# Kernel optimization log

Measured on AMD Instinct MI355X. Metric: run time of the kernel, lower is better.

The kernel has to match this reference:

```python
import jax, jax.numpy as jnp
import numpy as np

B, H, W, D, L, M = 16, 256, 256, 32, 4, 12  # batch, grid H, grid W, d_model, num_layers, modes
BN_EPS = 1e-5


def setup_inputs() -> dict:
    key = jax.random.key(0)
    ks = jax.random.split(key, 12)
    scale = 1.0 / (D * D)  # SpectralConv2d init scale: 1/(in_ch*out_ch)
    return {
        "x": jax.random.normal(ks[0], (B, H, W), jnp.float32),
        "coords_x": jax.random.uniform(ks[1], (1, 2, 1, H, W), dtype=jnp.float32),
        # linear_in: 3 -> D
        "w_in": jax.random.normal(ks[2], (D, 3), jnp.float32) * 0.3,
        "b_in": jnp.zeros((D,), jnp.float32),
        # per-layer spectral weights (real/imag), torch.rand-style uniform [0,1)*scale
        "w1r": jax.random.uniform(ks[3], (L, D, D, M, M), dtype=jnp.float32) * scale,
        "w1i": jax.random.uniform(ks[4], (L, D, D, M, M), dtype=jnp.float32) * scale,
        "w2r": jax.random.uniform(ks[5], (L, D, D, M, M), dtype=jnp.float32) * scale,
        "w2i": jax.random.uniform(ks[6], (L, D, D, M, M), dtype=jnp.float32) * scale,
        # per-layer pointwise linear D -> D
        "lw": jax.random.normal(ks[7], (L, D, D), jnp.float32) * (1.0 / np.sqrt(D)),
        "lb": jnp.zeros((L, D), jnp.float32),
        # per-layer BatchNorm affine params
        "gamma": jnp.ones((L, D), jnp.float32),
        "beta": jnp.zeros((L, D), jnp.float32),
        # linear_out: D -> 1
        "w_out": jax.random.normal(ks[8], (1, D), jnp.float32) * (1.0 / np.sqrt(D)),
        "b_out": jnp.zeros((1,), jnp.float32),
    }


def _fourier_layer(h, w1, w2, lw, lb, gamma, beta):
    # h: [B, D, H, W]
    Bh, C, Hh, Wh = h.shape
    h_ft = jnp.fft.rfft2(h)  # [B, D, H, W//2+1] complex64
    # low-mode truncation + complex channel mixing on two corner blocks
    top = jnp.einsum('bixy,ioxy->boxy', h_ft[:, :, :M, :M], w1)
    bot = jnp.einsum('bixy,ioxy->boxy', h_ft[:, :, Hh - M:, :M], w2)
    out_ft = jnp.zeros((Bh, C, Hh, Wh // 2 + 1), jnp.complex64)
    out_ft = out_ft.at[:, :, :M, :M].set(top).at[:, :, Hh - M:, :M].set(bot)
    y = jnp.fft.irfft2(out_ft, s=(Hh, Wh))  # [B, D, H, W]
    # residual pointwise linear (x + Linear(x)), then ReLU, then BatchNorm2d (batch stats)
    y = y + jnp.einsum('bchw,oc->bohw', y, lw) + lb[None, :, None, None]
    y = jax.nn.relu(y)
    mean = y.mean(axis=(0, 2, 3), keepdims=True)
    var = y.var(axis=(0, 2, 3), keepdims=True)
    y = (y - mean) * jax.lax.rsqrt(var + BN_EPS)
    return y * gamma[None, :, None, None] + beta[None, :, None, None]


def reference(x, coords_x, w_in, b_in, w1r, w1i, w2r, w2i, lw, lb, gamma, beta, w_out, b_out):
    # coords_x: [1,2,1,H,W] -> squeeze dim 2 -> broadcast to [B,2,H,W]
    cx = jnp.broadcast_to(coords_x[:, :, 0], (x.shape[0], 2, H, W))
    h = jnp.concatenate([x[:, None], cx], axis=1)  # [B, 3, H, W]
    h = jnp.einsum('bchw,dc->bdhw', h, w_in) + b_in[None, :, None, None]  # linear_in
    for i in range(L):  # fixed small layer count
        h = _fourier_layer(h, w1r[i] + 1j * w1i[i], w2r[i] + 1j * w2i[i],
                           lw[i], lb[i], gamma[i], beta[i])
    out = jnp.einsum('bdhw,od->bohw', h, w_out) + b_out[None, :, None, None]  # linear_out
    return out[:, 0]  # [B, H, W]
```

## Files before the change

kernel.cpp:

```cpp
#include <hip/hip_runtime.h>

constexpr double PI2 = 6.283185307179586476925286766559;
constexpr float INV_HW = 1.0f / 65536.0f;


__global__ __launch_bounds__(256) void k_init(float* __restrict__ cs,
                                              float* __restrict__ Tg) {
  int t = threadIdx.x;
  double a = PI2 * (double)t / 256.0;
  cs[2*t]   = (float)cos(a);
  cs[2*t+1] = (float)sin(a);
  for (int i = t; i < 1536; i += 256) {
    int k = i >> 7, xs = i & 127;
    double ang = PI2 * (double)(k * xs) / 256.0;
    Tg[i]        = (float)cos(ang);
    Tg[1536 + i] = (float)sin(ang);
  }
  for (int i = t; i < 176; i += 256) {
    int k = (i >> 4) + 1, j = i & 15;
    double ang = PI2 * (double)(k * j) / 256.0;
    Tg[3072 + i] = (float)cos(ang);
    Tg[3248 + i] = (float)sin(ang);
  }
}

__global__ __launch_bounds__(256) void k_prep(
    const float* __restrict__ w1r, const float* __restrict__ w1i,
    const float* __restrict__ w2r, const float* __restrict__ w2i,
    const float* __restrict__ lw, float* __restrict__ wf)
{
  const int bid = blockIdx.x;
  const int l = bid / 288, m = bid % 288;
  const int ky = m / 12, kx = m % 12;
  const int kyp = (ky < 12) ? ky : ky - 12;
  const float* wr_ = ((ky < 12) ? w1r : w2r) + l*147456;
  const float* wi_ = ((ky < 12) ? w1i : w2i) + l*147456;
  __shared__ float wre[1024], wim[1024], lwl[1024];
  const int tid = threadIdx.x;
  for (int f = tid; f < 1024; f += 256) {
    int idx = f*144 + kyp*12 + kx;
    wre[f] = wr_[idx]; wim[f] = wi_[idx];
    lwl[f] = lw[l*1024 + f];
  }
  __syncthreads();
  float* o_ = wf + (long)bid*2048;
  for (int f = tid; f < 1024; f += 256) {
    int i = f >> 5, o = f & 31;
    float ar = wre[f], ai = wim[f];
    #pragma unroll
    for (int c = 0; c < 32; ++c) {
      float lv = lwl[o*32 + c];
      ar += wre[i*32 + c] * lv;
      ai += wim[i*32 + c] * lv;
    }
    o_[f] = ar; o_[1024 + f] = ai;
  }
}

__global__ __launch_bounds__(256) void k_embed_fwd(
    const float* __restrict__ xin, const float* __restrict__ coords,
    const float* __restrict__ w_in, const float* __restrict__ b_in,
    const float* __restrict__ Tg, float* __restrict__ gxo)
{
  __shared__ float wl[96], bl[32];
  __shared__ __align__(16) float E[32*132];
  __shared__ __align__(16) float O[32*132];
  const int tid = threadIdx.x;
  if (tid < 96) wl[tid] = w_in[tid];
  if (tid >= 96 && tid < 128) bl[tid-96] = b_in[tid-96];
  const int b = blockIdx.x >> 8, y = blockIdx.x & 255;
  const int xs = tid & 127, half = tid >> 7;
  const int cbase = half << 4;
  const int xhi = (256 - xs) & 255;
  const float xvL = xin[(b*256 + y)*256 + xs];
  const float c0L = coords[y*256 + xs];
  const float c1L = coords[65536 + y*256 + xs];
  const float xvH = xin[(b*256 + y)*256 + xhi];
  const float c0H = coords[y*256 + xhi];
  const float c1H = coords[65536 + y*256 + xhi];
  __syncthreads();
  #pragma unroll
  for (int cc = 0; cc < 16; ++cc) {
    const int c = cbase + cc;
    float lo = wl[3*c]*xvL + wl[3*c+1]*c0L + wl[3*c+2]*c1L + bl[c];
    float hi = wl[3*c]*xvH + wl[3*c+1]*c0H + wl[3*c+2]*c1H + bl[c];
    E[c*132 + xs] = (xs == 0) ? lo : (lo + hi);
    O[c*132 + xs] = (xs == 0) ? 0.f : (lo - hi);
  }
  if (tid < 32) {
    const int c = tid;
    const float xv = xin[(b*256 + y)*256 + 128];
    const float c0 = coords[y*256 + 128];
    const float c1 = coords[65536 + y*256 + 128];
    E[c*132 + 128] = wl[3*c]*xv + wl[3*c+1]*c0 + wl[3*c+2]*c1 + bl[c];
  }
  __syncthreads();
  const int wv = tid >> 6, lane = tid & 63;
  const int seg = lane >> 3, chl = lane & 7;
  const int ch = wv*8 + chl;
  const float* Erow = &E[ch*132 + seg*16];
  const float* Orow = &O[ch*132 + seg*16];
  const float* T2c = Tg + 3072;
  const float* T2s = Tg + 3248;
  float A[11], Bv[11], Cc[11], Dd[11];
  #pragma unroll
  for (int k = 0; k < 11; ++k) { A[k]=0.f; Bv[k]=0.f; Cc[k]=0.f; Dd[k]=0.f; }
  float s0 = 0.f;
  #pragma unroll
  for (int c4 = 0; c4 < 4; ++c4) {
    float4 E4 = *(const float4*)(Erow + 4*c4);
    float4 O4 = *(const float4*)(Orow + 4*c4);
    float ej[4] = {E4.x, E4.y, E4.z, E4.w};
    float oj[4] = {O4.x, O4.y, O4.z, O4.w};
    #pragma unroll
    for (int jj = 0; jj < 4; ++jj) {
      const int j = 4*c4 + jj;
      const float e = ej[jj], o = oj[jj];
      s0 += e;
      #pragma unroll
      for (int k = 0; k < 11; ++k) {
        const float ckj = T2c[k*16 + j];
        const float skj = T2s[k*16 + j];
        A[k]  += e*ckj;
        Bv[k] += e*skj;
        Dd[k] += o*ckj;
        Cc[k] += o*skj;
      }
    }
  }
  float arr[12], aii[12];
  arr[0] = s0; aii[0] = 0.f;
  #pragma unroll
  for (int k = 1; k < 12; ++k) {
    const float twc = Tg[k*128 + seg*16];
    const float tws = Tg[1536 + k*128 + seg*16];
    arr[k] = A[k-1]*twc - Bv[k-1]*tws;
    aii[k] = -(Cc[k-1]*twc + Dd[k-1]*tws);
  }
  #pragma unroll
  for (int k = 0; k < 12; ++k) {
    arr[k] += __shfl_xor(arr[k], 8, 64);
    arr[k] += __shfl_xor(arr[k], 16, 64);
    arr[k] += __shfl_xor(arr[k], 32, 64);
  }
  #pragma unroll
  for (int k = 1; k < 12; ++k) {
    aii[k] += __shfl_xor(aii[k], 8, 64);
    aii[k] += __shfl_xor(aii[k], 16, 64);
    aii[k] += __shfl_xor(aii[k], 32, 64);
  }
  {
    const float e128 = E[ch*132 + 128];
    float* gp = gxo + ((long)(b*256 + y)*32 + ch)*24;
    #pragma unroll
    for (int j = 0; j < 3; ++j) {
      const int v = seg*3 + j;
      if (v < 12) {
        float s = arr[v] + ((v & 1) ? -e128 : e128);
        gp[2*v] = s;
        if (v == 0) gp[1] = 0.f;
      } else if (v < 23) {
        gp[2*(v - 11) + 1] = aii[v - 11];
      }
    }
  }
}

__global__ __launch_bounds__(512) void k_spec(
    const float* __restrict__ gx, const float* __restrict__ cs,
    const float* __restrict__ bnp, const float* __restrict__ wfl,
    float* __restrict__ gy)
{
  const int bid = (blockIdx.x % 8) * 24 + blockIdx.x / 8;
  const int b = bid / 12, kx = bid % 12;
  __shared__ float2 Z[32*257];
  __shared__ float fcl[24*66];
  __shared__ float fml[24*66];
  __shared__ __align__(16) float csl[512];
  const int tid = threadIdx.x;
  if (tid < 512) csl[tid] = cs[tid];
  {
    const int ch = tid & 31;
    float sc = 1.0f, badd = 0.0f;
    if (bnp) { sc = bnp[ch]; if (kx == 0) badd = 256.0f * bnp[32 + ch]; }
    const float* src = gx + ((long)(b*256)*32 + ch)*24 + 2*kx;
    const int ybase = tid >> 5;
    #pragma unroll
    for (int i = 0; i < 16; ++i) {
      int y = ybase + 16*i;
      float2 v = *(const float2*)(src + (long)y*768);
      float2 w; w.x = sc*v.x + badd; w.y = sc*v.y;
      Z[ch*257 + y] = w;
    }
  }
  __syncthreads();
  for (int t = tid; t < 832; t += 512) {
    const int hf = t & 1, r = t >> 1;
    const int pr = r % 13, ch = r / 13;
    const int kyv = (pr <= 10) ? (pr + 1) : ((pr == 11) ? 0 : 244);
    const int y0 = hf << 7;
    int tt = (kyv * y0) & 255;
    float A = 0.f, Bv = 0.f, C2 = 0.f, D = 0.f;
    const float2* Zp = &Z[ch*257 + y0];
    for (int i = 0; i < 128; ++i) {
      float2 v = Zp[i];
      float2 w = *(const float2*)&csl[2*tt];
      A  += v.x*w.x;  D  += v.x*w.y;
      C2 += v.y*w.x;  Bv += v.y*w.y;
      tt = (tt + kyv) & 255;
    }
    A  += __shfl_xor(A, 1, 64);
    Bv += __shfl_xor(Bv, 1, 64);
    C2 += __shfl_xor(C2, 1, 64);
    D  += __shfl_xor(D, 1, 64);
    if (hf == 0) {
      const int slo = (pr <= 10) ? (pr + 1) : ((pr == 11) ? 0 : 12);
      fcl[slo*66 + 2*ch]     = A + Bv;
      fcl[slo*66 + 2*ch + 1] = C2 - D;
      if (pr <= 10) {
        fcl[(23 - pr)*66 + 2*ch]     = A - Bv;
        fcl[(23 - pr)*66 + 2*ch + 1] = C2 + D;
      }
    }
  }
  __syncthreads();
  for (int t = tid; t < 768; t += 512) {
    const int ky = t >> 5, o = t & 31;
    const float* wb = wfl + ((long)(ky*12 + kx))*2048;
    const float* fr = &fcl[ky*66];
    float ar = 0.f, ai = 0.f;
    #pragma unroll
    for (int i = 0; i < 32; ++i) {
      float fre = fr[2*i], fim = fr[2*i+1];
      float wr = wb[i*32 + o], wi = wb[1024 + i*32 + o];
      ar += fre*wr - fim*wi;
      ai += fre*wi + fim*wr;
    }
    fml[ky*66 + 2*o]     = ar;
    fml[ky*66 + 2*o + 1] = ai;
  }
  __syncthreads();
  {
    const int yp = tid & 127, og = tid >> 7;
    float tc[24], tsn[24];
    #pragma unroll
    for (int s = 0; s < 24; ++s) {
      int kyv = (s < 12) ? s : (232 + s);
      int tt = (kyv * yp) & 255;
      tc[s] = csl[2*tt]; tsn[s] = csl[2*tt+1];
    }
    const int yhi = (256 - yp) & 255;
    float* rowLo = gy + ((long)(b*256 + yp))*768 + kx*64;
    float* rowHi = gy + ((long)(b*256 + yhi))*768 + kx*64;
    #pragma unroll
    for (int oo = 0; oo < 8; oo += 2) {
      const int o = og*8 + oo;
      float A1a=0.f,A2a=0.f,A3a=0.f,A4a=0.f;
      float A1b=0.f,A2b=0.f,A3b=0.f,A4b=0.f;
      #pragma unroll
      for (int s = 0; s < 24; ++s) {
        float fra = fml[s*66 + 2*o],     fia = fml[s*66 + 2*o + 1];
        float frb = fml[s*66 + 2*o + 2], fib = fml[s*66 + 2*o + 3];
        float c = tc[s], sn = tsn[s];
        A1a += fra*c;  A2a += fia*sn;  A3a += fra*sn;  A4a += fia*c;
        A1b += frb*c;  A2b += fib*sn;  A3b += frb*sn;  A4b += fib*c;
      }
      float4 lo, hi;
      lo.x = (A1a - A2a)*INV_HW; lo.y = (A3a + A4a)*INV_HW;
      lo.z = (A1b - A2b)*INV_HW; lo.w = (A3b + A4b)*INV_HW;
      hi.x = (A1a + A2a)*INV_HW; hi.y = (A4a - A3a)*INV_HW;
      hi.z = (A1b + A2b)*INV_HW; hi.w = (A4b - A3b)*INV_HW;
      *(float4*)(rowLo + 2*o) = lo;
      *(float4*)(rowHi + 2*o) = hi;
    }
  }
  if (tid < 32) {
    const int o = tid;
    float re = 0.f, im = 0.f;
    #pragma unroll
    for (int s = 0; s < 24; ++s) {
      float fr = fml[s*66 + 2*o], fi = fml[s*66 + 2*o + 1];
      if (s & 1) { re -= fr; im -= fi; } else { re += fr; im += fi; }
    }
    float* row = gy + ((long)(b*256 + 128))*768 + kx*64;
    row[2*o]     = re*INV_HW;
    row[2*o + 1] = im*INV_HW;
  }
}

__global__ __launch_bounds__(256) void k_fuse(
    const float* __restrict__ gy, const float* __restrict__ Tg,
    const float* __restrict__ lb,
    float* __restrict__ gxo, float* __restrict__ part, float* __restrict__ z)
{
  const int b = blockIdx.x >> 8, y = blockIdx.x & 255;
  const int tid = threadIdx.x;
  __shared__ __align__(16) float E[32*132];
  __shared__ __align__(16) float O[32*132];
  const int xs = tid & 127, half = tid >> 7;
  const int cbase = half << 4;
  const int xhi = (256 - xs) & 255;
  float tc[12], tsn[12];
  #pragma unroll
  for (int kx = 1; kx < 12; ++kx) {
    tc[kx]  = 2.0f * Tg[kx*128 + xs];
    tsn[kx] = 2.0f * Tg[1536 + kx*128 + xs];
  }
  const float* Gg = gy + (long)(b*256 + y)*768;
  float zlo[16], zhi[16];
  #pragma unroll
  for (int cc = 0; cc < 16; cc += 2) {
    const int c = cbase + cc;
    float base0 = Gg[2*c], base1 = Gg[2*c + 2];
    float cos0 = 0.f, sin0 = 0.f, cos1 = 0.f, sin1 = 0.f;
    #pragma unroll
    for (int kx = 1; kx < 12; ++kx) {
      float4 g = *(const float4*)(Gg + kx*64 + 2*c);
      cos0 += g.x*tc[kx];  sin0 += g.y*tsn[kx];
      cos1 += g.z*tc[kx];  sin1 += g.w*tsn[kx];
    }
    const float l0 = lb[c], l1 = lb[c+1];
    zlo[cc]   = fmaxf(base0 + cos0 - sin0 + l0, 0.f);
    zhi[cc]   = fmaxf(base0 + cos0 + sin0 + l0, 0.f);
    zlo[cc+1] = fmaxf(base1 + cos1 - sin1 + l1, 0.f);
    zhi[cc+1] = fmaxf(base1 + cos1 + sin1 + l1, 0.f);
  }
  #pragma unroll
  for (int cc = 0; cc < 16; ++cc) {
    float e = (xs == 0) ? zlo[cc] : (zlo[cc] + zhi[cc]);
    float o = (xs == 0) ? 0.f     : (zlo[cc] - zhi[cc]);
    E[(cbase+cc)*132 + xs] = e;
    O[(cbase+cc)*132 + xs] = o;
  }
  if (z) {
    #pragma unroll
    for (int cc = 0; cc < 16; ++cc) {
      z[((b*32 + cbase+cc)*256 + y)*256 + xs]  = zlo[cc];
      z[((b*32 + cbase+cc)*256 + y)*256 + xhi] = zhi[cc];
    }
  }
  if (tid < 32) {
    const int c = tid;
    float acc = Gg[2*c] + lb[c];
    #pragma unroll
    for (int kx = 1; kx < 12; ++kx) {
      float2 g = *(const float2*)(Gg + kx*64 + 2*c);
      acc += (kx & 1) ? (-2.0f * g.x) : (2.0f * g.x);
    }
    float zv = fmaxf(acc, 0.f);
    E[c*132 + 128] = zv;
    if (z) z[((b*32 + c)*256 + y)*256 + 128] = zv;
  }
  __syncthreads();
  const int wv = tid >> 6, lane = tid & 63;
  const int seg = lane >> 3, chl = lane & 7;
  const int ch = wv*8 + chl;
  const float* Erow = &E[ch*132 + seg*16];
  const float* Orow = &O[ch*132 + seg*16];
  float arr[12], aii[12], sq = 0.f;
  if (gxo) {
    const float* T2c = Tg + 3072;
    const float* T2s = Tg + 3248;
    float A[11], Bv[11], Cc[11], Dd[11];
    #pragma unroll
    for (int k = 0; k < 11; ++k) { A[k]=0.f; Bv[k]=0.f; Cc[k]=0.f; Dd[k]=0.f; }
    float s0 = 0.f;
    #pragma unroll
    for (int c4 = 0; c4 < 4; ++c4) {
      float4 E4 = *(const float4*)(Erow + 4*c4);
      float4 O4 = *(const float4*)(Orow + 4*c4);
      float ej[4] = {E4.x, E4.y, E4.z, E4.w};
      float oj[4] = {O4.x, O4.y, O4.z, O4.w};
      #pragma unroll
      for (int jj = 0; jj < 4; ++jj) {
        const int j = 4*c4 + jj;
        const float e = ej[jj], o = oj[jj];
        s0 += e;
        sq += e*e + o*o;
        #pragma unroll
        for (int k = 0; k < 11; ++k) {
          const float ckj = T2c[k*16 + j];
          const float skj = T2s[k*16 + j];
          A[k]  += e*ckj;
          Bv[k] += e*skj;
          Dd[k] += o*ckj;
          Cc[k] += o*skj;
        }
      }
    }
    arr[0] = s0; aii[0] = 0.f;
    #pragma unroll
    for (int k = 1; k < 12; ++k) {
      const float twc = Tg[k*128 + seg*16];
      const float tws = Tg[1536 + k*128 + seg*16];
      arr[k] = A[k-1]*twc - Bv[k-1]*tws;
      aii[k] = -(Cc[k-1]*twc + Dd[k-1]*tws);
    }
  } else {
    #pragma unroll
    for (int k = 0; k < 12; ++k) { arr[k]=0.f; aii[k]=0.f; }
    #pragma unroll
    for (int c4 = 0; c4 < 4; ++c4) {
      float4 E4 = *(const float4*)(Erow + 4*c4);
      float4 O4 = *(const float4*)(Orow + 4*c4);
      arr[0] += E4.x + E4.y + E4.z + E4.w;
      sq += E4.x*E4.x + E4.y*E4.y + E4.z*E4.z + E4.w*E4.w
          + O4.x*O4.x + O4.y*O4.y + O4.z*O4.z + O4.w*O4.w;
    }
  }
  #pragma unroll
  for (int k = 0; k < 12; ++k) {
    arr[k] += __shfl_xor(arr[k], 8, 64);
    arr[k] += __shfl_xor(arr[k], 16, 64);
    arr[k] += __shfl_xor(arr[k], 32, 64);
  }
  if (gxo) {
    #pragma unroll
    for (int k = 1; k < 12; ++k) {
      aii[k] += __shfl_xor(aii[k], 8, 64);
      aii[k] += __shfl_xor(aii[k], 16, 64);
      aii[k] += __shfl_xor(aii[k], 32, 64);
    }
  }
  sq += __shfl_xor(sq, 8, 64);
  sq += __shfl_xor(sq, 16, 64);
  sq += __shfl_xor(sq, 32, 64);
  {
    const float e0   = E[ch*132];
    const float e128 = E[ch*132 + 128];
    float* gp = gxo ? (gxo + ((long)(b*256 + y)*32 + ch)*24) : nullptr;
    #pragma unroll
    for (int j = 0; j < 3; ++j) {
      const int v = seg*3 + j;
      if (v < 12) {
        float s = arr[v] + ((v & 1) ? -e128 : e128);
        if (gp) {
          gp[2*v] = s;
          if (v == 0) gp[1] = 0.f;
        }
        if (v == 0) part[(long)blockIdx.x*64 + 2*ch] = s;
      } else if (v < 23) {
        if (gp) gp[2*(v - 11) + 1] = aii[v - 11];
      } else {
        part[(long)blockIdx.x*64 + 2*ch + 1] = 0.5f*sq + 0.5f*e0*e0 + e128*e128;
      }
    }
  }
}

__global__ __launch_bounds__(256) void k_stats(
    const float* __restrict__ part, const float* __restrict__ gamma,
    const float* __restrict__ beta, float* __restrict__ bn)
{
  const int c = blockIdx.x, tid = threadIdx.x;
  float s1 = 0.f, s2 = 0.f;
  for (int j = tid; j < 4096; j += 256) {
    s1 += part[(long)j*64 + 2*c];
    s2 += part[(long)j*64 + 2*c + 1];
  }
  #pragma unroll
  for (int d = 32; d; d >>= 1) {
    s1 += __shfl_xor(s1, d, 64);
    s2 += __shfl_xor(s2, d, 64);
  }
  __shared__ float r1[4], r2[4];
  int w = tid >> 6;
  if ((tid & 63) == 0) { r1[w] = s1; r2[w] = s2; }
  __syncthreads();
  if (tid == 0) {
    float S1 = r1[0]+r1[1]+r1[2]+r1[3];
    float S2 = r2[0]+r2[1]+r2[2]+r2[3];
    const float N = 1048576.0f;
    float mean = S1 / N;
    float var  = S2 / N - mean*mean;
    float inv  = rsqrtf(var + 1e-5f);
    float sc   = gamma[c] * inv;
    bn[c]      = sc;
    bn[32 + c] = beta[c] - mean*sc;
  }
}

__global__ __launch_bounds__(256) void k_out(
    const float* __restrict__ z, const float* __restrict__ bn,
    const float* __restrict__ w_out, const float* __restrict__ b_out,
    float* __restrict__ out)
{
  __shared__ float a[32];
  __shared__ float c0s;
  const int tid = threadIdx.x;
  if (tid < 32) a[tid] = bn[tid] * w_out[tid];
  if (tid == 0) {
    float t = b_out[0];
    for (int c = 0; c < 32; ++c) t += bn[32 + c] * w_out[c];
    c0s = t;
  }
  __syncthreads();
  int gid = blockIdx.x*256 + tid;
  int b = gid >> 14, pos = (gid & 16383) << 2;
  const float* zb = z + (long)b*2097152 + pos;
  float c0 = c0s;
  float r0 = c0, r1 = c0, r2 = c0, r3 = c0;
  #pragma unroll 8
  for (int c = 0; c < 32; ++c) {
    float4 v = *(const float4*)(zb + c*65536);
    float ac = a[c];
    r0 += v.x*ac; r1 += v.y*ac; r2 += v.z*ac; r3 += v.w*ac;
  }
  float4 res; res.x = r0; res.y = r1; res.z = r2; res.w = r3;
  *(float4*)(out + (long)b*65536 + pos) = res;
}

extern "C" void kernel_launch(void* const* d_in, const int* in_sizes, int n_in,
                              void* d_out, int out_size, void* d_ws, size_t ws_size,
                              hipStream_t stream) {
  const float* x      = (const float*)d_in[0];
  const float* coords = (const float*)d_in[1];
  const float* w_in   = (const float*)d_in[2];
  const float* b_in   = (const float*)d_in[3];
  const float* w1r    = (const float*)d_in[4];
  const float* w1i    = (const float*)d_in[5];
  const float* w2r    = (const float*)d_in[6];
  const float* w2i    = (const float*)d_in[7];
  const float* lw     = (const float*)d_in[8];
  const float* lb     = (const float*)d_in[9];
  const float* gamma  = (const float*)d_in[10];
  const float* beta   = (const float*)d_in[11];
  const float* w_out  = (const float*)d_in[12];
  const float* b_out  = (const float*)d_in[13];
  float* out = (float*)d_out;
  float* ws  = (float*)d_ws;

  float* cs   = ws;
  float* z    = cs + 512;
  float* gx   = z;
  float* wf   = z + 3145728;
  float* gy   = z + 33554432;
  float* part = gy + 3145728;
  float* Tg   = part + 294912;
  float* bn   = Tg + 294912;

  k_init<<<1, 256, 0, stream>>>(cs, Tg);
  k_prep<<<1152, 256, 0, stream>>>(w1r, w1i, w2r, w2i, lw, wf);
  k_embed_fwd<<<4096, 256, 0, stream>>>(x, coords, w_in, b_in, Tg, gx);

  for (int l = 0; l < 4; ++l) {
    k_spec<<<192, 512, 0, stream>>>(gx, cs, (l == 0) ? nullptr : bn,
                                    wf + (long)l*589824, gy);
    k_fuse<<<4096, 256, 0, stream>>>(gy, Tg, lb + l*32,
                                     (l < 3) ? gx : nullptr, part,
                                     (l == 3) ? z : nullptr);
    k_stats<<<32, 256, 0, stream>>>(part, gamma + l*32, beta + l*32, bn);
  }

  k_out<<<1024, 256, 0, stream>>>(z, bn, w_out, b_out, out);
}
```

Measured before the change: 484.2 us.

## Split spectral kernel into forward-DFT and mixing/inverse kernels with more blocks

The single 192-block spectral kernel becomes two kernels of 768 blocks each. The first does the y-direction forward DFT per channel group and writes the truncated coefficients to a global buffer. The second reloads them, does the complex channel mixing, and computes the inverse y-DFT for a quarter of the rows. The aim is to fill the GPU's many compute units better than 192 blocks could. In exchange it adds a launch and a global round trip per layer, and the channel-mixing work is repeated in each of the four quarter blocks.

Result: no change. 478.9 us (-1.1%).

```diff
diff --git a/kernel.cpp b/kernel.cpp
--- a/kernel.cpp
+++ b/kernel.cpp
@@ -166,42 +166,42 @@
   }
 }
 
-__global__ __launch_bounds__(512) void k_spec(
+__global__ __launch_bounds__(256) void k_sf(
     const float* __restrict__ gx, const float* __restrict__ cs,
-    const float* __restrict__ bnp, const float* __restrict__ wfl,
-    float* __restrict__ gy)
-{
-  const int bid = (blockIdx.x % 8) * 24 + blockIdx.x / 8;
-  const int b = bid / 12, kx = bid % 12;
-  __shared__ float2 Z[32*257];
-  __shared__ float fcl[24*66];
-  __shared__ float fml[24*66];
+    const float* __restrict__ bnp, float* __restrict__ fc)
+{
+  const int bid = (blockIdx.x % 8) * 96 + blockIdx.x / 8;
+  const int chg = bid & 3;
+  const int kx = (bid >> 2) % 12;
+  const int b = bid / 48;
+  __shared__ float2 Z[8*257];
   __shared__ __align__(16) float csl[512];
   const int tid = threadIdx.x;
-  if (tid < 512) csl[tid] = cs[tid];
+  for (int f = tid; f < 512; f += 256) csl[f] = cs[f];
   {
-    const int ch = tid & 31;
+    const int chl = tid & 7;
+    const int ch = chg*8 + chl;
     float sc = 1.0f, badd = 0.0f;
     if (bnp) { sc = bnp[ch]; if (kx == 0) badd = 256.0f * bnp[32 + ch]; }
     const float* src = gx + ((long)(b*256)*32 + ch)*24 + 2*kx;
-    const int ybase = tid >> 5;
-    #pragma unroll
-    for (int i = 0; i < 16; ++i) {
-      int y = ybase + 16*i;
+    const int ybase = tid >> 3;
+    #pragma unroll
+    for (int i = 0; i < 8; ++i) {
+      int y = ybase + 32*i;
       float2 v = *(const float2*)(src + (long)y*768);
       float2 w; w.x = sc*v.x + badd; w.y = sc*v.y;
-      Z[ch*257 + y] = w;
-    }
-  }
-  __syncthreads();
-  for (int t = tid; t < 832; t += 512) {
-    const int hf = t & 1, r = t >> 1;
-    const int pr = r % 13, ch = r / 13;
+      Z[chl*257 + y] = w;
+    }
+  }
+  __syncthreads();
+  if (tid < 208) {
+    const int hf = tid & 1, r = tid >> 1;
+    const int pr = r % 13, chl = r / 13;
     const int kyv = (pr <= 10) ? (pr + 1) : ((pr == 11) ? 0 : 244);
     const int y0 = hf << 7;
     int tt = (kyv * y0) & 255;
     float A = 0.f, Bv = 0.f, C2 = 0.f, D = 0.f;
-    const float2* Zp = &Z[ch*257 + y0];
+    const float2* Zp = &Z[chl*257 + y0];
     for (int i = 0; i < 128; ++i) {
       float2 v = Zp[i];
       float2 w = *(const float2*)&csl[2*tt];
@@ -214,17 +214,37 @@
     C2 += __shfl_xor(C2, 1, 64);
     D  += __shfl_xor(D, 1, 64);
     if (hf == 0) {
+      const int ch = chg*8 + chl;
       const int slo = (pr <= 10) ? (pr + 1) : ((pr == 11) ? 0 : 12);
-      fcl[slo*66 + 2*ch]     = A + Bv;
-      fcl[slo*66 + 2*ch + 1] = C2 - D;
+      float* o1 = fc + ((b*24 + slo)*12 + kx)*64 + 2*ch;
+      o1[0] = A + Bv; o1[1] = C2 - D;
       if (pr <= 10) {
-        fcl[(23 - pr)*66 + 2*ch]     = A - Bv;
-        fcl[(23 - pr)*66 + 2*ch + 1] = C2 + D;
+        float* o2 = fc + ((b*24 + (23 - pr))*12 + kx)*64 + 2*ch;
+        o2[0] = A - Bv; o2[1] = C2 + D;
       }
     }
   }
-  __syncthreads();
-  for (int t = tid; t < 768; t += 512) {
+}
+
+__global__ __launch_bounds__(256) void k_mi(
+    const float* __restrict__ fc, const float* __restrict__ cs,
+    const float* __restrict__ wfl, float* __restrict__ gy)
+{
+  const int bid = (blockIdx.x % 8) * 96 + blockIdx.x / 8;
+  const int q = bid & 3;
+  const int kx = (bid >> 2) % 12;
+  const int b = bid / 48;
+  __shared__ float fcl[24*66];
+  __shared__ float fml[24*66];
+  __shared__ __align__(16) float csl[512];
+  const int tid = threadIdx.x;
+  for (int f = tid; f < 512; f += 256) csl[f] = cs[f];
+  for (int f = tid; f < 1536; f += 256) {
+    int ky = f >> 6, j = f & 63;
+    fcl[ky*66 + j] = fc[((b*24 + ky)*12 + kx)*64 + j];
+  }
+  __syncthreads();
+  for (int t = tid; t < 768; t += 256) {
     const int ky = t >> 5, o = t & 31;
     const float* wb = wfl + ((long)(ky*12 + kx))*2048;
     const float* fr = &fcl[ky*66];
@@ -241,7 +261,7 @@
   }
   __syncthreads();
   {
-    const int yp = tid & 127, og = tid >> 7;
+    const int yp = q*32 + (tid & 31), og = tid >> 5;
     float tc[24], tsn[24];
     #pragma unroll
     for (int s = 0; s < 24; ++s) {
@@ -253,8 +273,8 @@
     float* rowLo = gy + ((long)(b*256 + yp))*768 + kx*64;
     float* rowHi = gy + ((long)(b*256 + yhi))*768 + kx*64;
     #pragma unroll
-    for (int oo = 0; oo < 8; oo += 2) {
-      const int o = og*8 + oo;
+    for (int oo = 0; oo < 4; oo += 2) {
+      const int o = og*4 + oo;
       float A1a=0.f,A2a=0.f,A3a=0.f,A4a=0.f;
       float A1b=0.f,A2b=0.f,A3b=0.f,A4b=0.f;
       #pragma unroll
@@ -274,7 +294,7 @@
       *(float4*)(rowHi + 2*o) = hi;
     }
   }
-  if (tid < 32) {
+  if (q == 3 && tid < 32) {
     const int o = tid;
     float re = 0.f, im = 0.f;
     #pragma unroll
@@ -534,6 +554,7 @@
   float* z    = cs + 512;
   float* gx   = z;
   float* wf   = z + 3145728;
+  float* fc   = z + 5505024;
   float* gy   = z + 33554432;
   float* part = gy + 3145728;
   float* Tg   = part + 294912;
@@ -544,8 +565,8 @@
   k_embed_fwd<<<4096, 256, 0, stream>>>(x, coords, w_in, b_in, Tg, gx);
 
   for (int l = 0; l < 4; ++l) {
-    k_spec<<<192, 512, 0, stream>>>(gx, cs, (l == 0) ? nullptr : bn,
-                                    wf + (long)l*589824, gy);
+    k_sf<<<768, 256, 0, stream>>>(gx, cs, (l == 0) ? nullptr : bn, fc);
+    k_mi<<<768, 256, 0, stream>>>(fc, cs, wf + (long)l*589824, gy);
     k_fuse<<<4096, 256, 0, stream>>>(gy, Tg, lb + l*32,
                                      (l < 3) ? gx : nullptr, part,
                                      (l == 3) ? z : nullptr);
```
